# Optimization experiments

Hardware: AMD Instinct MI355X
Metric: run time of the kernel (lower is better)

Reference implementation:

```python
import jax, jax.numpy as jnp
import numpy as np
from jax import lax

B, C, T = 64, 122, 500
COUT, D, H, FF, L = 64, 128, 8, 256, 2
NSUB, NCLS = 13, 4
EPS = 1e-5


def _gelu(x):
    return jax.nn.gelu(x, approximate=False)  # torch nn.GELU default (erf)


def _bn(x, g, b, m, v):
    # eval-mode BatchNorm1d over channel dim of [N, C, T]
    scale = (g / jnp.sqrt(v + EPS))[None, :, None]
    return (x - m[None, :, None]) * scale + b[None, :, None]


def _ln(x, g, b):
    mu = x.mean(-1, keepdims=True)
    var = ((x - mu) ** 2).mean(-1, keepdims=True)
    return (x - mu) / jnp.sqrt(var + EPS) * g + b


def _conv1d(x, w, b, pad):
    y = lax.conv_general_dilated(x, w, (1,), [(pad, pad)], dimension_numbers=('NCH', 'OIH', 'NCH'))
    return y + b[None, :, None]


def forward(x, subject_ids, conv1_w, conv1_b, bn1_g, bn1_b, bn1_m, bn1_v,
            conv2_w, conv2_b, bn2_g, bn2_b, bn2_m, bn2_v,
            proj_w, proj_b, elec_emb,
            qkv_w, qkv_b, out_w, out_b, ln1_g, ln1_b,
            ff1_w, ff1_b, ff2_w, ff2_b, ln2_g, ln2_b,
            heads_w, heads_b):
    bsz = x.shape[0]
    h = x.reshape(bsz * C, 1, T)                               # [B*C, 1, T]
    h = _gelu(_bn(_conv1d(h, conv1_w, conv1_b, 4), bn1_g, bn1_b, bn1_m, bn1_v))
    h = h.reshape(bsz * C, COUT, T // 2, 2).max(-1)            # MaxPool1d(2)
    h = _gelu(_bn(_conv1d(h, conv2_w, conv2_b, 2), bn2_g, bn2_b, bn2_m, bn2_v))
    h = h.mean(-1)                                             # AdaptiveAvgPool1d(1)
    tok = h @ proj_w.T + proj_b                                # [B*C, D]
    tok = tok.reshape(bsz, C, D) + elec_emb[:, :C, :]
    dh = D // H
    inv_sqrt_dh = 1.0 / float(np.sqrt(dh))
    for l in range(L):  # post-norm TransformerEncoderLayer, gelu activation
        qkv = jnp.einsum('bsd,ed->bse', tok, qkv_w[l]) + qkv_b[l]
        q, k, v = jnp.split(qkv, 3, axis=-1)
        q = q.reshape(bsz, C, H, dh)
        k = k.reshape(bsz, C, H, dh)
        v = v.reshape(bsz, C, H, dh)
        att = jax.nn.softmax(jnp.einsum('bqhd,bkhd->bhqk', q, k) * inv_sqrt_dh, axis=-1)
        ctx = jnp.einsum('bhqk,bkhd->bqhd', att, v).reshape(bsz, C, D)
        tok = _ln(tok + ctx @ out_w[l].T + out_b[l], ln1_g[l], ln1_b[l])
        ff = _gelu(tok @ ff1_w[l].T + ff1_b[l]) @ ff2_w[l].T + ff2_b[l]
        tok = _ln(tok + ff, ln2_g[l], ln2_b[l])
    pooled = tok.mean(axis=1)                                  # [B, D]
    # per-subject head routing == gather subject's weight/bias, batched matvec
    hw = heads_w[subject_ids]                                  # [B, NCLS, D]
    hb = heads_b[subject_ids]                                  # [B, NCLS]
    return jnp.einsum('bd,bcd->bc', pooled, hw) + hb


def setup_inputs() -> dict:
    key = jax.random.key(0)
    ks = jax.random.split(key, 16)
    def n(i, shape, s=0.02):
        return jax.random.normal(ks[i], shape, jnp.float32) * s
    return {
        'x': jax.random.normal(ks[0], (B, C, T), jnp.float32),
        'subject_ids': jax.random.randint(ks[1], (B,), 0, NSUB),
        'conv1_w': n(2, (COUT, 1, 9), 0.3), 'conv1_b': jnp.zeros((COUT,), jnp.float32),
        'bn1_g': jnp.ones((COUT,), jnp.float32), 'bn1_b': jnp.zeros((COUT,), jnp.float32),
        'bn1_m': jnp.zeros((COUT,), jnp.float32), 'bn1_v': jnp.ones((COUT,), jnp.float32),
        'conv2_w': n(3, (COUT, COUT, 5), 0.05), 'conv2_b': jnp.zeros((COUT,), jnp.float32),
        'bn2_g': jnp.ones((COUT,), jnp.float32), 'bn2_b': jnp.zeros((COUT,), jnp.float32),
        'bn2_m': jnp.zeros((COUT,), jnp.float32), 'bn2_v': jnp.ones((COUT,), jnp.float32),
        'proj_w': n(4, (D, COUT), 0.05), 'proj_b': jnp.zeros((D,), jnp.float32),
        'elec_emb': n(5, (1, C, D), 0.02),
        'qkv_w': n(6, (L, 3 * D, D), 0.05), 'qkv_b': jnp.zeros((L, 3 * D), jnp.float32),
        'out_w': n(7, (L, D, D), 0.05), 'out_b': jnp.zeros((L, D), jnp.float32),
        'ln1_g': jnp.ones((L, D), jnp.float32), 'ln1_b': jnp.zeros((L, D), jnp.float32),
        'ff1_w': n(8, (L, FF, D), 0.05), 'ff1_b': jnp.zeros((L, FF), jnp.float32),
        'ff2_w': n(9, (L, D, FF), 0.05), 'ff2_b': jnp.zeros((L, D), jnp.float32),
        'ln2_g': jnp.ones((L, D), jnp.float32), 'ln2_b': jnp.zeros((L, D), jnp.float32),
        'heads_w': n(10, (NSUB, NCLS, D), 0.05), 'heads_b': jnp.zeros((NSUB, NCLS), jnp.float32),
    }


def reference(x, subject_ids, conv1_w, conv1_b, bn1_g, bn1_b, bn1_m, bn1_v,
              conv2_w, conv2_b, bn2_g, bn2_b, bn2_m, bn2_v,
              proj_w, proj_b, elec_emb,
              qkv_w, qkv_b, out_w, out_b, ln1_g, ln1_b,
              ff1_w, ff1_b, ff2_w, ff2_b, ln2_g, ln2_b,
              heads_w, heads_b):
    return forward(x, subject_ids, conv1_w, conv1_b, bn1_g, bn1_b, bn1_m, bn1_v,
                   conv2_w, conv2_b, bn2_g, bn2_b, bn2_m, bn2_v,
                   proj_w, proj_b, elec_emb,
                   qkv_w, qkv_b, out_w, out_b, ln1_g, ln1_b,
                   ff1_w, ff1_b, ff2_w, ff2_b, ln2_g, ln2_b,
                   heads_w, heads_b)
```

## Files before the change

### kernel.cpp

```cpp
#include <hip/hip_runtime.h>
#include <hip/hip_fp16.h>
#include <hip/hip_bf16.h>
#include <math.h>

#define BB 64
#define CC 122
#define TT 500
#define NCOUT 64
#define DD 128
#define HHEADS 8
#define FFDIM 256
#define NLAYER 2
#define EPS 1e-5f
#define SEQ (BB*CC)

#define WS_W2T     0u
#define WS_S1      20480u
#define WS_SH1     20544u
#define WS_S2      20608u
#define WS_SH2     20672u
#define WS_WBF     20736u
#define WS_TOK     151808u
#define WS_QKVB    1151232u
#define WS_VTB     2150656u
#define WS_GTAB    2674944u
#define WS_W1S     2675968u
#define WS_QKVB2   2676992u
#define WS_VTB2    3676416u

#define WB_QKV  0u
#define WB_OUT  98304u
#define WB_FF1  131072u
#define WB_FF2  196608u

typedef __attribute__((ext_vector_type(8))) short bf16x8;
typedef __attribute__((ext_vector_type(4))) float f32x4;

__device__ __forceinline__ unsigned short f2bf(float f) {
    unsigned int u = __float_as_uint(f);
    unsigned int r = u + 0x7FFFu + ((u >> 16) & 1u);
    return (unsigned short)(r >> 16);
}

__device__ __forceinline__ float gelu_fast(float x) {
    float z = fabsf(x) * 0.70710678118654752f;
    float t = __builtin_amdgcn_rcpf(fmaf(0.3275911f, z, 1.0f));
    float p = fmaf(fmaf(fmaf(fmaf(1.061405429f, t, -1.453152027f), t,
                             1.421413741f), t, -0.284496736f), t, 0.254829592f);
    float e = __expf(-z * z);
    float erf_abs = fmaf(-p * t, e, 1.0f);
    float erf_x = copysignf(erf_abs, x);
    return 0.5f * x * (1.0f + erf_x);
}

__device__ __forceinline__ float gelu_tab(float x, const unsigned* __restrict__ gt) {
    float p = fmaf(x, 32.0f, 256.0f);
    p = fminf(fmaxf(p, 0.0f), 511.999f);
    int i = (int)p;
    float fr = p - (float)i;
    unsigned u = gt[i];
    __half2 h2 = *(__half2*)&u;
    float v0 = __half2float(h2.x);
    float d  = __half2float(h2.y);
    return fmaf(fr, d, v0);
}

__global__ void prep_kernel(const float* __restrict__ conv1_w, const float* __restrict__ conv1_b,
                            const float* __restrict__ bn1_g, const float* __restrict__ bn1_b,
                            const float* __restrict__ bn1_m, const float* __restrict__ bn1_v,
                            const float* __restrict__ conv2_w, const float* __restrict__ conv2_b,
                            const float* __restrict__ bn2_g, const float* __restrict__ bn2_b,
                            const float* __restrict__ bn2_m, const float* __restrict__ bn2_v,
                            const float* __restrict__ qkv_w, const float* __restrict__ out_w,
                            const float* __restrict__ ff1_w, const float* __restrict__ ff2_w,
                            float* __restrict__ ws) {
    int idx = blockIdx.x * blockDim.x + threadIdx.x;
    if (idx < 20480) {
        int ci = idx & 63; int co = (idx >> 6) & 63; int kk = idx >> 12;
        unsigned short* wt = (unsigned short*)(ws + WS_W2T);
        wt[idx] = f2bf(conv2_w[(co*64 + ci)*5 + kk]);
    } else if (idx < 20544) {
        int i = idx - 20480;
        float s = bn1_g[i] * rsqrtf(bn1_v[i] + EPS);
        ws[WS_S1 + i] = s;
        ws[WS_SH1 + i] = (conv1_b[i] - bn1_m[i]) * s + bn1_b[i];
    } else if (idx < 20608) {
        int i = idx - 20544;
        float s = bn2_g[i] * rsqrtf(bn2_v[i] + EPS);
        ws[WS_S2 + i] = s;
        ws[WS_SH2 + i] = (conv2_b[i] - bn2_m[i]) * s + bn2_b[i];
    } else if (idx < 282752) {
        int r = idx - 20608;
        unsigned short* wbf = (unsigned short*)(ws + WS_WBF);
        float v;
        if (r < 98304)       v = qkv_w[r];
        else if (r < 131072) v = out_w[r - 98304];
        else if (r < 196608) v = ff1_w[r - 131072];
        else                 v = ff2_w[r - 196608];
        wbf[r] = f2bf(v);
    } else if (idx < 283264) {
        int i = idx - 282752;
        float x0 = (i - 256) * 0.03125f;
        float x1 = x0 + 0.03125f;
        float g0 = 0.5f*x0*(1.0f + erff(x0*0.70710678118654752f));
        float g1 = 0.5f*x1*(1.0f + erff(x1*0.70710678118654752f));
        __half hv = __float2half_rn(g0);
        __half hd = __float2half_rn(g1 - g0);
        unsigned short uv = *(unsigned short*)&hv;
        unsigned short ud = *(unsigned short*)&hd;
        ((unsigned*)(ws + WS_GTAB))[i] = (unsigned)uv | ((unsigned)ud << 16);
    } else if (idx < 285312) {
        int i = idx - 283264;
        int co = i >> 5, k = i & 31;
        unsigned short* w1s = (unsigned short*)(ws + WS_W1S);
        float s = bn1_g[co] * rsqrtf(bn1_v[co] + EPS);
        w1s[i] = (k < 9) ? f2bf(conv1_w[co*9 + k] * s) : (unsigned short)0;
    }
}

__global__ __launch_bounds__(256, 4) void conv_kernel(const float* __restrict__ x,
            const float* __restrict__ proj_w, const float* __restrict__ proj_b,
            const float* __restrict__ elec,
            const float* __restrict__ wsr, float* __restrict__ tok) {
    __shared__ __align__(16) unsigned short h1s[264*64];
    __shared__ __align__(16) unsigned short xbf[544];
    __shared__ __align__(16) unsigned gtab[512];
    __shared__ float part[256];
    __shared__ float mean_l[64];
    int n = blockIdx.x;
    int c = n % CC;
    int tid = threadIdx.x;
    const float* xg = x + (size_t)n * TT;

    for (int i = tid; i < 544; i += 256) {
        unsigned short v = 0;
        if (i >= 4 && i < 504) v = f2bf(xg[i-4]);
        xbf[i] = v;
    }
    if (tid < 128) {
        ((uint4*)gtab)[tid] = ((const uint4*)(wsr + WS_GTAB))[tid];
    }
    for (int idx = tid; idx < 14*64; idx += 256) {
        int rr = idx >> 6;
        int r = (rr < 2) ? rr : (rr - 2 + 252);
        h1s[r*64 + (idx & 63)] = 0;
    }
    __syncthreads();

    int lane = tid & 63;
    int w = tid >> 6;
    int ln15 = lane & 15, lg = lane >> 4;

    {
        const unsigned short* w1s = (const unsigned short*)(wsr + WS_W1S);
        bf16x8 b1f[4];
        float sh1v[4];
#pragma unroll
        for (int nt = 0; nt < 4; nt++) {
            int co = nt*16 + ln15;
            b1f[nt] = *(const bf16x8*)&w1s[co*32 + lg*8];
            sh1v[nt] = wsr[WS_SH1 + co];
        }
        for (int mi = 0; mi < 8; mi++) {
            int mt = w*8 + mi;
            int t = mt*16 + ln15;
            short e[8];
#pragma unroll
            for (int j = 0; j < 8; j++) e[j] = (short)xbf[t + lg*8 + j];
            bf16x8 af = {e[0],e[1],e[2],e[3],e[4],e[5],e[6],e[7]};
#pragma unroll
            for (int nt = 0; nt < 4; nt++) {
                f32x4 cacc = __builtin_amdgcn_mfma_f32_16x16x32_bf16(af, b1f[nt],
                                (f32x4){0.f,0.f,0.f,0.f}, 0, 0, 0);
                float g0 = gelu_tab(cacc[0] + sh1v[nt], gtab);
                float g1 = gelu_tab(cacc[1] + sh1v[nt], gtab);
                float g2 = gelu_tab(cacc[2] + sh1v[nt], gtab);
                float g3 = gelu_tab(cacc[3] + sh1v[nt], gtab);
                int tpA = mt*8 + lg*2;
                if (tpA < 250) {
                    int co = nt*16 + ln15;
                    union { __hip_bfloat162 b; unsigned u; } pk;
                    pk.b = __float22bfloat162_rn(make_float2(fmaxf(g0, g1), fmaxf(g2, g3)));
                    int r = tpA + 2;
                    int cp = (co >> 3) ^ (r & 7);
                    h1s[r*64 + cp*8 + (co & 7)] = (unsigned short)(pk.u & 0xffffu);
                    int r2 = r + 1;
                    int cp2 = (co >> 3) ^ (r2 & 7);
                    h1s[r2*64 + cp2*8 + (co & 7)] = (unsigned short)(pk.u >> 16);
                }
            }
        }
    }
    __syncthreads();

    const unsigned short* wt = (const unsigned short*)(wsr + WS_W2T);
    f32x4 acc[4][4];
#pragma unroll
    for (int mi = 0; mi < 4; mi++)
#pragma unroll
        for (int nt = 0; nt < 4; nt++) acc[mi][nt] = (f32x4){0.f, 0.f, 0.f, 0.f};

    const unsigned short* wbase = wt + ln15*64 + lg*8;
#pragma unroll
    for (int kk = 0; kk < 5; kk++) {
#pragma unroll
        for (int s = 0; s < 2; s++) {
            bf16x8 bfv[4];
#pragma unroll
            for (int nt = 0; nt < 4; nt++)
                bfv[nt] = *(const bf16x8*)(wbase + kk*4096 + nt*1024 + s*32);
#pragma unroll
            for (int mi = 0; mi < 4; mi++) {
                int r = (w*4 + mi)*16 + ln15 + kk;
                int cp = (s*4 + lg) ^ (r & 7);
                bf16x8 af = *(const bf16x8*)&h1s[r*64 + cp*8];
#pragma unroll
                for (int nt = 0; nt < 4; nt++)
                    acc[mi][nt] = __builtin_amdgcn_mfma_f32_16x16x32_bf16(af, bfv[nt], acc[mi][nt], 0, 0, 0);
            }
        }
    }

#pragma unroll
    for (int nt = 0; nt < 4; nt++) {
        int co2 = nt*16 + ln15;
        float sc = wsr[WS_S2 + co2], sh = wsr[WS_SH2 + co2];
        float p = 0.f;
#pragma unroll
        for (int mi = 0; mi < 4; mi++) {
            int tbase = (w*4 + mi)*16 + lg*4;
#pragma unroll
            for (int i = 0; i < 4; i++) {
                if (tbase + i < 250)
                    p += gelu_tab(fmaf(acc[mi][nt][i], sc, sh), gtab);
            }
        }
        p += __shfl_down(p, 32, 64);
        p += __shfl_down(p, 16, 64);
        if (lane < 16) part[w*64 + co2] = p;
    }
    __syncthreads();
    if (tid < 64) {
        mean_l[tid] = (part[tid] + part[64+tid] + part[128+tid] + part[192+tid]) * (1.0f/250.0f);
    }
    __syncthreads();

    if (tid < DD) {
        int d = tid;
        float a = proj_b[d] + elec[c*DD + d];
#pragma unroll 8
        for (int o = 0; o < 64; o++) a = fmaf(mean_l[o], proj_w[d*64 + o], a);
        tok[(size_t)n * DD + d] = a;
    }
}

__global__ __launch_bounds__(256) void qkv_gemm(const float* __restrict__ Aptr,
        const unsigned short* __restrict__ Bbf,
        const float* __restrict__ bias,
        unsigned short* __restrict__ qkvb,
        unsigned short* __restrict__ vtb) {
    const int tid = threadIdx.x;
    const int m0 = blockIdx.x * 32;
    const int y  = blockIdx.y;
    const int n0 = y * 128;
    __shared__ __align__(16) unsigned short As[32*128];

    const float* A = Aptr + (size_t)m0 * 128;
    for (int i = tid; i < 1024; i += 256) {
        int m = i >> 5; int kq = (i & 31)*4;
        float4 v = *(const float4*)(A + m*128 + kq);
        int cp = (kq >> 3) ^ (m & 15);
        short4 s4 = make_short4((short)f2bf(v.x), (short)f2bf(v.y),
                                (short)f2bf(v.z), (short)f2bf(v.w));
        *(short4*)&As[m*128 + cp*8 + (kq & 7)] = s4;
    }
    __syncthreads();

    const int lane = tid & 63, w = tid >> 6;
    const int ln15 = lane & 15, lg = lane >> 4;
    f32x4 acc[2][2];
#pragma unroll
    for (int mi = 0; mi < 2; mi++)
#pragma unroll
        for (int ni = 0; ni < 2; ni++) acc[mi][ni] = (f32x4){0.f, 0.f, 0.f, 0.f};

    const unsigned short* Bb = Bbf + (size_t)n0 * 128;
#pragma unroll
    for (int kt = 0; kt < 4; kt++) {
        bf16x8 af[2], bfv[2];
#pragma unroll
        for (int mi = 0; mi < 2; mi++) {
            int m = mi*16 + ln15;
            int cp = (kt*4 + lg) ^ (m & 15);
            af[mi] = *(const bf16x8*)&As[m*128 + cp*8];
        }
#pragma unroll
        for (int ni = 0; ni < 2; ni++) {
            int nn = (w*2 + ni)*16 + ln15;
            bfv[ni] = *(const bf16x8*)&Bb[(size_t)nn*128 + kt*32 + lg*8];
        }
#pragma unroll
        for (int mi = 0; mi < 2; mi++)
#pragma unroll
            for (int ni = 0; ni < 2; ni++)
                acc[mi][ni] = __builtin_amdgcn_mfma_f32_16x16x32_bf16(af[mi], bfv[ni], acc[mi][ni], 0, 0, 0);
    }

#pragma unroll
    for (int mi = 0; mi < 2; mi++)
#pragma unroll
        for (int ni = 0; ni < 2; ni++) {
            int nloc = (w*2 + ni)*16 + ln15;
            float bb = bias[n0 + nloc];
#pragma unroll
            for (int i = 0; i < 4; i++) {
                int ml = mi*16 + lg*4 + i;
                int nrow = m0 + ml;
                unsigned short us = f2bf(acc[mi][ni][i] + bb);
                if (y < 2) {
                    qkvb[(size_t)nrow*256 + n0 + nloc] = us;
                } else {
                    int bq = nrow / 122;
                    int j  = nrow - bq*122;
                    vtb[((size_t)(bq*128 + nloc))*128 + j] = us;
                }
            }
        }
}

__global__ __launch_bounds__(512) void attn_tail(
        const unsigned short* __restrict__ qkvb,
        const unsigned short* __restrict__ vtb,
        const unsigned short* __restrict__ outW, const float* __restrict__ outb,
        float* __restrict__ tok,
        const float* __restrict__ ln1g, const float* __restrict__ ln1b,
        const unsigned short* __restrict__ B1, const float* __restrict__ b1,
        const unsigned short* __restrict__ B2, const float* __restrict__ b2,
        const float* __restrict__ ln2g, const float* __restrict__ ln2b,
        const unsigned short* __restrict__ Bq, const float* __restrict__ bq,
        unsigned short* __restrict__ qkvb_o, unsigned short* __restrict__ vtb_o,
        int do_qkv) {
    __shared__ float Cs[32*129];
    __shared__ __align__(16) unsigned short Pregion[8*16*128];
    __shared__ __align__(16) unsigned short ctxs[32*128];

    const int tid = threadIdx.x;
    const int blk = blockIdx.x;
    const int b = blk >> 2, mq = blk & 3;
    const int m0l = mq * 32;
    const int lane = tid & 63, w = tid >> 6;
    const int ln15 = lane & 15, lg = lane >> 4;

    const unsigned short* qb = qkvb + (size_t)b * 122 * 256;
    unsigned short* Pw = Pregion + w * 2048;

    {
        const int h = w;
#pragma unroll
        for (int mt = 0; mt < 2; mt++) {
            int mrow = m0l + mt*16 + ln15;
            int gr = (mrow < 122) ? mrow : 121;
            bf16x8 af = {0,0,0,0,0,0,0,0};
            if (lg < 2) af = *(const bf16x8*)(qb + gr*256 + h*16 + lg*8);
            f32x4 S[8];
#pragma unroll
            for (int nt = 0; nt < 8; nt++) {
                int j = nt*16 + ln15;
                int gj = (j < 122) ? j : 121;
                bf16x8 bv = {0,0,0,0,0,0,0,0};
                if (lg < 2) bv = *(const bf16x8*)(qb + gj*256 + 128 + h*16 + lg*8);
                S[nt] = __builtin_amdgcn_mfma_f32_16x16x32_bf16(af, bv,
                            (f32x4){0.f,0.f,0.f,0.f}, 0, 0, 0);
            }
            float sm[4];
#pragma unroll
            for (int i = 0; i < 4; i++) {
                float m_ = -1e30f;
#pragma unroll
                for (int nt = 0; nt < 8; nt++) {
                    float v = S[nt][i] * 0.25f;
                    if (nt == 7 && ln15 >= 10) v = -1e30f;
                    S[nt][i] = v;
                    m_ = fmaxf(m_, v);
                }
                m_ = fmaxf(m_, __shfl_xor(m_, 1, 64));
                m_ = fmaxf(m_, __shfl_xor(m_, 2, 64));
                m_ = fmaxf(m_, __shfl_xor(m_, 4, 64));
                m_ = fmaxf(m_, __shfl_xor(m_, 8, 64));
                float s_ = 0.f;
#pragma unroll
                for (int nt = 0; nt < 8; nt++) {
                    float e = __expf(S[nt][i] - m_);
                    S[nt][i] = e;
                    s_ += e;
                }
                s_ += __shfl_xor(s_, 1, 64);
                s_ += __shfl_xor(s_, 2, 64);
                s_ += __shfl_xor(s_, 4, 64);
                s_ += __shfl_xor(s_, 8, 64);
                sm[i] = s_;
            }
#pragma unroll
            for (int nt = 0; nt < 8; nt++)
#pragma unroll
                for (int i = 0; i < 4; i++) {
                    int rp = lg*4 + i;
                    int j = nt*16 + ln15;
                    int cp = (j >> 3) ^ rp;
                    Pw[rp*128 + cp*8 + (j & 7)] = f2bf(S[nt][i]);
                }
            f32x4 cacc = (f32x4){0.f,0.f,0.f,0.f};
#pragma unroll
            for (int kt = 0; kt < 4; kt++) {
                bf16x8 bv = *(const bf16x8*)(vtb + ((size_t)(b*128 + h*16 + ln15))*128 + kt*32 + lg*8);
                int m = ln15;
                int cp = (kt*4 + lg) ^ m;
                bf16x8 ap = *(const bf16x8*)&Pw[m*128 + cp*8];
                cacc = __builtin_amdgcn_mfma_f32_16x16x32_bf16(ap, bv, cacc, 0, 0, 0);
            }
#pragma unroll
            for (int i = 0; i < 4; i++) {
                float inv = __builtin_amdgcn_rcpf(sm[i]);
                int rp = mt*16 + lg*4 + i;
                int ccol = h*16 + ln15;
                int cp = (ccol >> 3) ^ (rp & 15);
                ctxs[rp*128 + cp*8 + (ccol & 7)] = f2bf(cacc[i] * inv);
            }
        }
    }
    __syncthreads();

    {
        f32x4 acc[2];
#pragma unroll
        for (int mi = 0; mi < 2; mi++) acc[mi] = (f32x4){0.f,0.f,0.f,0.f};
        int nn = w*16 + ln15;
#pragma unroll
        for (int kt = 0; kt < 4; kt++) {
            bf16x8 bv = *(const bf16x8*)&outW[(size_t)nn*128 + kt*32 + lg*8];
#pragma unroll
            for (int mi = 0; mi < 2; mi++) {
                int m = mi*16 + ln15;
                int cp = (kt*4 + lg) ^ (m & 15);
                bf16x8 afm = *(const bf16x8*)&ctxs[m*128 + cp*8];
                acc[mi] = __builtin_amdgcn_mfma_f32_16x16x32_bf16(afm, bv, acc[mi], 0, 0, 0);
            }
        }
        float bb = outb[nn];
#pragma unroll
        for (int mi = 0; mi < 2; mi++)
#pragma unroll
            for (int i = 0; i < 4; i++) {
                int ml = mi*16 + lg*4 + i;
                int mrow = m0l + ml;
                int grow = b*122 + ((mrow < 122) ? mrow : 121);
                Cs[ml*129 + nn] = acc[mi][i] + bb + tok[(size_t)grow*128 + nn];
            }
    }
    __syncthreads();

    unsigned short* ln1buf = Pregion;
    unsigned short* Hs = Pregion + 4096;
    {
        int r = tid >> 4, sub = tid & 15;
        float s1 = 0.f, s2 = 0.f;
#pragma unroll
        for (int j = 0; j < 8; j++) {
            float vv = Cs[r*129 + sub*8 + j];
            s1 += vv; s2 += vv*vv;
        }
        s1 += __shfl_xor(s1, 1, 64); s2 += __shfl_xor(s2, 1, 64);
        s1 += __shfl_xor(s1, 2, 64); s2 += __shfl_xor(s2, 2, 64);
        s1 += __shfl_xor(s1, 4, 64); s2 += __shfl_xor(s2, 4, 64);
        s1 += __shfl_xor(s1, 8, 64); s2 += __shfl_xor(s2, 8, 64);
        float mu = s1 * (1.0f/128.0f);
        float var = s2 * (1.0f/128.0f) - mu*mu;
        float rstd = rsqrtf(var + EPS);
#pragma unroll
        for (int j = 0; j < 8; j++) {
            int nloc = sub*8 + j;
            float vv = (Cs[r*129 + nloc] - mu) * rstd * ln1g[nloc] + ln1b[nloc];
            Cs[r*129 + nloc] = vv;
            int cp = (nloc >> 3) ^ (r & 15);
            ln1buf[r*128 + cp*8 + (nloc & 7)] = f2bf(vv);
        }
    }
    __syncthreads();

    {
        f32x4 acc1[2][2];
#pragma unroll
        for (int mi = 0; mi < 2; mi++)
#pragma unroll
            for (int ni = 0; ni < 2; ni++) acc1[mi][ni] = (f32x4){0.f,0.f,0.f,0.f};
#pragma unroll
        for (int kt = 0; kt < 4; kt++) {
            bf16x8 afm[2];
#pragma unroll
            for (int mi = 0; mi < 2; mi++) {
                int m = mi*16 + ln15;
                int cp = (kt*4 + lg) ^ (m & 15);
                afm[mi] = *(const bf16x8*)&ln1buf[m*128 + cp*8];
            }
#pragma unroll
            for (int ni = 0; ni < 2; ni++) {
                int nn = (w*2 + ni)*16 + ln15;
                bf16x8 bv = *(const bf16x8*)&B1[(size_t)nn*128 + kt*32 + lg*8];
#pragma unroll
                for (int mi = 0; mi < 2; mi++)
                    acc1[mi][ni] = __builtin_amdgcn_mfma_f32_16x16x32_bf16(afm[mi], bv, acc1[mi][ni], 0, 0, 0);
            }
        }
#pragma unroll
        for (int ni = 0; ni < 2; ni++) {
            int nn = (w*2 + ni)*16 + ln15;
            float bb = b1[nn];
#pragma unroll
            for (int mi = 0; mi < 2; mi++)
#pragma unroll
                for (int i = 0; i < 4; i++) {
                    int m = mi*16 + lg*4 + i;
                    float v = gelu_fast(acc1[mi][ni][i] + bb);
                    int cp = (nn >> 3) ^ (m & 15);
                    Hs[m*256 + cp*8 + (nn & 7)] = f2bf(v);
                }
        }
    }
    __syncthreads();

    {
        f32x4 acc2[2];
#pragma unroll
        for (int mi = 0; mi < 2; mi++) acc2[mi] = (f32x4){0.f,0.f,0.f,0.f};
        int nn = w*16 + ln15;
#pragma unroll
        for (int kt = 0; kt < 8; kt++) {
            bf16x8 bv = *(const bf16x8*)&B2[(size_t)nn*256 + kt*32 + lg*8];
#pragma unroll
            for (int mi = 0; mi < 2; mi++) {
                int m = mi*16 + ln15;
                int cp = (kt*4 + lg) ^ (m & 15);
                bf16x8 afm = *(const bf16x8*)&Hs[m*256 + cp*8];
                acc2[mi] = __builtin_amdgcn_mfma_f32_16x16x32_bf16(afm, bv, acc2[mi], 0, 0, 0);
            }
        }
        float bb = b2[nn];
#pragma unroll
        for (int mi = 0; mi < 2; mi++)
#pragma unroll
            for (int i = 0; i < 4; i++) {
                int ml = mi*16 + lg*4 + i;
                Cs[ml*129 + nn] = acc2[mi][i] + bb + Cs[ml*129 + nn];
            }
    }
    __syncthreads();

    {
        int r = tid >> 4, sub = tid & 15;
        float s1 = 0.f, s2 = 0.f;
#pragma unroll
        for (int j = 0; j < 8; j++) {
            float vv = Cs[r*129 + sub*8 + j];
            s1 += vv; s2 += vv*vv;
        }
        s1 += __shfl_xor(s1, 1, 64); s2 += __shfl_xor(s2, 1, 64);
        s1 += __shfl_xor(s1, 2, 64); s2 += __shfl_xor(s2, 2, 64);
        s1 += __shfl_xor(s1, 4, 64); s2 += __shfl_xor(s2, 4, 64);
        s1 += __shfl_xor(s1, 8, 64); s2 += __shfl_xor(s2, 8, 64);
        float mu = s1 * (1.0f/128.0f);
        float var = s2 * (1.0f/128.0f) - mu*mu;
        float rstd = rsqrtf(var + EPS);
        bool rowok = (m0l + r < 122);
#pragma unroll
        for (int j = 0; j < 8; j++) {
            int nloc = sub*8 + j;
            float vv = (Cs[r*129 + nloc] - mu) * rstd * ln2g[nloc] + ln2b[nloc];
            if (rowok)
                tok[((size_t)(b*122 + m0l + r))*128 + nloc] = vv;
            if (do_qkv) {
                int cp = (nloc >> 3) ^ (r & 15);
                Pregion[r*128 + cp*8 + (nloc & 7)] = f2bf(vv);
            }
        }
    }

    if (do_qkv) {
        __syncthreads();
        const unsigned short* qbuf = Pregion;
        f32x4 accq[2][3];
#pragma unroll
        for (int mi = 0; mi < 2; mi++)
#pragma unroll
            for (int ni = 0; ni < 3; ni++) accq[mi][ni] = (f32x4){0.f,0.f,0.f,0.f};
#pragma unroll
        for (int kt = 0; kt < 4; kt++) {
            bf16x8 afm[2];
#pragma unroll
            for (int mi = 0; mi < 2; mi++) {
                int m = mi*16 + ln15;
                int cp = (kt*4 + lg) ^ (m & 15);
                afm[mi] = *(const bf16x8*)&qbuf[m*128 + cp*8];
            }
#pragma unroll
            for (int ni = 0; ni < 3; ni++) {
                int e = w*48 + ni*16 + ln15;
                bf16x8 bv = *(const bf16x8*)&Bq[(size_t)e*128 + kt*32 + lg*8];
#pragma unroll
                for (int mi = 0; mi < 2; mi++)
                    accq[mi][ni] = __builtin_amdgcn_mfma_f32_16x16x32_bf16(afm[mi], bv, accq[mi][ni], 0, 0, 0);
            }
        }
#pragma unroll
        for (int ni = 0; ni < 3; ni++) {
            int e = w*48 + ni*16 + ln15;
            float bb = bq[e];
#pragma unroll
            for (int mi = 0; mi < 2; mi++)
#pragma unroll
                for (int i = 0; i < 4; i++) {
                    int ml = mi*16 + lg*4 + i;
                    int mrow = m0l + ml;
                    if (mrow < 122) {
                        unsigned short us = f2bf(accq[mi][ni][i] + bb);
                        int nrow = b*122 + mrow;
                        if (e < 256)
                            qkvb_o[(size_t)nrow*256 + e] = us;
                        else
                            vtb_o[((size_t)(b*128 + (e - 256)))*128 + mrow] = us;
                    }
                }
        }
    }
}

__global__ __launch_bounds__(128) void final_kernel(const float* __restrict__ tok,
        const int* __restrict__ sid,
        const float* __restrict__ hw, const float* __restrict__ hb,
        float* __restrict__ outp) {
    __shared__ float pool[DD];
    int b = blockIdx.x, tid = threadIdx.x;
    float s = 0.f;
    for (int c2 = 0; c2 < CC; c2++) s += tok[((size_t)b*CC + c2)*DD + tid];
    pool[tid] = s * (1.0f/(float)CC);
    __syncthreads();
    if (tid < 4) {
        int sb = sid[b];
        const float* w = hw + ((size_t)sb*4 + tid)*DD;
        float a = hb[sb*4 + tid];
#pragma unroll 8
        for (int d = 0; d < DD; d++) a = fmaf(pool[d], w[d], a);
        outp[b*4 + tid] = a;
    }
}

extern "C" void kernel_launch(void* const* d_in, const int* in_sizes, int n_in,
                              void* d_out, int out_size, void* d_ws, size_t ws_size,
                              hipStream_t stream) {
    const float* x       = (const float*)d_in[0];
    const int*   sid     = (const int*)  d_in[1];
    const float* conv1_w = (const float*)d_in[2];
    const float* conv1_b = (const float*)d_in[3];
    const float* bn1_g   = (const float*)d_in[4];
    const float* bn1_b   = (const float*)d_in[5];
    const float* bn1_m   = (const float*)d_in[6];
    const float* bn1_v   = (const float*)d_in[7];
    const float* conv2_w = (const float*)d_in[8];
    const float* conv2_b = (const float*)d_in[9];
    const float* bn2_g   = (const float*)d_in[10];
    const float* bn2_b   = (const float*)d_in[11];
    const float* bn2_m   = (const float*)d_in[12];
    const float* bn2_v   = (const float*)d_in[13];
    const float* proj_w  = (const float*)d_in[14];
    const float* proj_b  = (const float*)d_in[15];
    const float* elec    = (const float*)d_in[16];
    const float* qkv_w   = (const float*)d_in[17];
    const float* qkv_b   = (const float*)d_in[18];
    const float* out_w   = (const float*)d_in[19];
    const float* out_b   = (const float*)d_in[20];
    const float* ln1_g   = (const float*)d_in[21];
    const float* ln1_b   = (const float*)d_in[22];
    const float* ff1_w   = (const float*)d_in[23];
    const float* ff1_b   = (const float*)d_in[24];
    const float* ff2_w   = (const float*)d_in[25];
    const float* ff2_b   = (const float*)d_in[26];
    const float* ln2_g   = (const float*)d_in[27];
    const float* ln2_b   = (const float*)d_in[28];
    const float* heads_w = (const float*)d_in[29];
    const float* heads_b = (const float*)d_in[30];
    float* ws = (float*)d_ws;
    const unsigned short* wbf = (const unsigned short*)(ws + WS_WBF);
    unsigned short* qkvb  = (unsigned short*)(ws + WS_QKVB);
    unsigned short* vtb   = (unsigned short*)(ws + WS_VTB);
    unsigned short* qkvb2 = (unsigned short*)(ws + WS_QKVB2);
    unsigned short* vtb2  = (unsigned short*)(ws + WS_VTB2);

    prep_kernel<<<(285312 + 255)/256, 256, 0, stream>>>(
        conv1_w, conv1_b, bn1_g, bn1_b, bn1_m, bn1_v,
        conv2_w, conv2_b, bn2_g, bn2_b, bn2_m, bn2_v,
        qkv_w, out_w, ff1_w, ff2_w, ws);

    conv_kernel<<<SEQ, 256, 0, stream>>>(x, proj_w, proj_b, elec, ws, ws + WS_TOK);

    qkv_gemm<<<dim3(244,3), 256, 0, stream>>>(
        ws + WS_TOK, wbf + WB_QKV, qkv_b, qkvb, vtb);

    attn_tail<<<BB*4, 512, 0, stream>>>(
        qkvb, vtb,
        wbf + WB_OUT, out_b,
        ws + WS_TOK, ln1_g, ln1_b,
        wbf + WB_FF1, ff1_b,
        wbf + WB_FF2, ff2_b,
        ln2_g, ln2_b,
        wbf + WB_QKV + 49152, qkv_b + 384, qkvb2, vtb2, 1);

    attn_tail<<<BB*4, 512, 0, stream>>>(
        qkvb2, vtb2,
        wbf + WB_OUT + 16384, out_b + 128,
        ws + WS_TOK, ln1_g + 128, ln1_b + 128,
        wbf + WB_FF1 + 32768, ff1_b + 256,
        wbf + WB_FF2 + 32768, ff2_b + 128,
        ln2_g + 128, ln2_b + 128,
        wbf + WB_QKV, qkv_b, qkvb2, vtb2, 0);

    final_kernel<<<BB, 128, 0, stream>>>(ws + WS_TOK, sid, heads_w, heads_b, (float*)d_out);
}
```

Measured before the change: 419.0 us.

## Restructure conv1 MFMA into even/odd pool pairs with hardware bf16 conversion

The conv1 stage now loads a register window of input once and builds even and odd shifted bf16 operands. It issues paired MFMAs so the max-pool combines matching output rows directly, instead of gathering eight scalar LDS reads per tile. The BN shift and the GELU table scale are folded into a single fma, and the h1s swizzle gains an extra XOR bit to cut LDS bank conflicts. Software round-to-nearest bf16 conversion is replaced throughout by the hardware v_cvt_pk_bf16_f32 instruction, which could differ slightly in NaN or rounding edge cases.

New measurement: 424.8 us. Within noise of the previous version (+1.4%).

```diff
diff --git a/kernel.cpp b/kernel.cpp
--- a/kernel.cpp
+++ b/kernel.cpp
@@ -42,6 +42,15 @@
     return (unsigned short)(r >> 16);
 }
 
+__device__ __forceinline__ unsigned pk_bf16(float a, float b) {
+    float r;
+    asm("v_cvt_pk_bf16_f32 %0, %1, %2" : "=v"(r) : "v"(a), "v"(b));
+    return __float_as_uint(r);
+}
+__device__ __forceinline__ unsigned short f2bf_hw(float f) {
+    return (unsigned short)pk_bf16(f, f);
+}
+
 __device__ __forceinline__ float gelu_fast(float x) {
     float z = fabsf(x) * 0.70710678118654752f;
     float t = __builtin_amdgcn_rcpf(fmaf(0.3275911f, z, 1.0f));
@@ -53,8 +62,7 @@
     return 0.5f * x * (1.0f + erf_x);
 }
 
-__device__ __forceinline__ float gelu_tab(float x, const unsigned* __restrict__ gt) {
-    float p = fmaf(x, 32.0f, 256.0f);
+__device__ __forceinline__ float gelu_idx(float p, const unsigned* __restrict__ gt) {
     p = fminf(fmaxf(p, 0.0f), 511.999f);
     int i = (int)p;
     float fr = p - (float)i;
@@ -134,7 +142,7 @@
 
     for (int i = tid; i < 544; i += 256) {
         unsigned short v = 0;
-        if (i >= 4 && i < 504) v = f2bf(xg[i-4]);
+        if (i >= 4 && i < 504) v = f2bf_hw(xg[i-4]);
         xbf[i] = v;
     }
     if (tid < 128) {
@@ -154,39 +162,46 @@
     {
         const unsigned short* w1s = (const unsigned short*)(wsr + WS_W1S);
         bf16x8 b1f[4];
-        float sh1v[4];
+        float shp[4];
 #pragma unroll
         for (int nt = 0; nt < 4; nt++) {
             int co = nt*16 + ln15;
             b1f[nt] = *(const bf16x8*)&w1s[co*32 + lg*8];
-            sh1v[nt] = wsr[WS_SH1 + co];
-        }
-        for (int mi = 0; mi < 8; mi++) {
-            int mt = w*8 + mi;
-            int t = mt*16 + ln15;
-            short e[8];
-#pragma unroll
-            for (int j = 0; j < 8; j++) e[j] = (short)xbf[t + lg*8 + j];
-            bf16x8 af = {e[0],e[1],e[2],e[3],e[4],e[5],e[6],e[7]};
+            shp[nt] = fmaf(wsr[WS_SH1 + co], 32.0f, 256.0f);
+        }
+        int P = w*128 + ln15*8 + lg*8;
+        uint4 Va = *(const uint4*)&xbf[P];
+        uint4 Vb = *(const uint4*)&xbf[P + 8];
+        unsigned vwin[8] = {Va.x, Va.y, Va.z, Va.w, Vb.x, Vb.y, Vb.z, Vb.w};
+#pragma unroll
+        for (int a = 0; a < 4; a++) {
+            union { unsigned u[4]; bf16x8 b; } Ue, Uo;
+#pragma unroll
+            for (int d = 0; d < 4; d++) {
+                Ue.u[d] = vwin[a + d];
+                Uo.u[d] = (vwin[a + d] >> 16) | (vwin[a + d + 1] << 16);
+            }
+            f32x4 ce[4], cod[4];
 #pragma unroll
             for (int nt = 0; nt < 4; nt++) {
-                f32x4 cacc = __builtin_amdgcn_mfma_f32_16x16x32_bf16(af, b1f[nt],
-                                (f32x4){0.f,0.f,0.f,0.f}, 0, 0, 0);
-                float g0 = gelu_tab(cacc[0] + sh1v[nt], gtab);
-                float g1 = gelu_tab(cacc[1] + sh1v[nt], gtab);
-                float g2 = gelu_tab(cacc[2] + sh1v[nt], gtab);
-                float g3 = gelu_tab(cacc[3] + sh1v[nt], gtab);
-                int tpA = mt*8 + lg*2;
-                if (tpA < 250) {
-                    int co = nt*16 + ln15;
-                    union { __hip_bfloat162 b; unsigned u; } pk;
-                    pk.b = __float22bfloat162_rn(make_float2(fmaxf(g0, g1), fmaxf(g2, g3)));
-                    int r = tpA + 2;
-                    int cp = (co >> 3) ^ (r & 7);
-                    h1s[r*64 + cp*8 + (co & 7)] = (unsigned short)(pk.u & 0xffffu);
-                    int r2 = r + 1;
-                    int cp2 = (co >> 3) ^ (r2 & 7);
-                    h1s[r2*64 + cp2*8 + (co & 7)] = (unsigned short)(pk.u >> 16);
+                ce[nt]  = __builtin_amdgcn_mfma_f32_16x16x32_bf16(Ue.b, b1f[nt],
+                              (f32x4){0.f,0.f,0.f,0.f}, 0, 0, 0);
+                cod[nt] = __builtin_amdgcn_mfma_f32_16x16x32_bf16(Uo.b, b1f[nt],
+                              (f32x4){0.f,0.f,0.f,0.f}, 0, 0, 0);
+            }
+#pragma unroll
+            for (int nt = 0; nt < 4; nt++) {
+                int co = nt*16 + ln15;
+#pragma unroll
+                for (int i = 0; i < 4; i++) {
+                    int tp = w*64 + lg*16 + i*4 + a;
+                    if (tp < 250) {
+                        float ge = gelu_idx(fmaf(ce[nt][i],  32.0f, shp[nt]), gtab);
+                        float go = gelu_idx(fmaf(cod[nt][i], 32.0f, shp[nt]), gtab);
+                        int r = tp + 2;
+                        int cp = (co >> 3) ^ (r & 7) ^ (((r >> 4) & 1) << 1);
+                        h1s[r*64 + cp*8 + (co & 7)] = f2bf_hw(fmaxf(ge, go));
+                    }
                 }
             }
         }
@@ -212,7 +227,7 @@
 #pragma unroll
             for (int mi = 0; mi < 4; mi++) {
                 int r = (w*4 + mi)*16 + ln15 + kk;
-                int cp = (s*4 + lg) ^ (r & 7);
+                int cp = (s*4 + lg) ^ (r & 7) ^ (((r >> 4) & 1) << 1);
                 bf16x8 af = *(const bf16x8*)&h1s[r*64 + cp*8];
 #pragma unroll
                 for (int nt = 0; nt < 4; nt++)
@@ -224,7 +239,8 @@
 #pragma unroll
     for (int nt = 0; nt < 4; nt++) {
         int co2 = nt*16 + ln15;
-        float sc = wsr[WS_S2 + co2], sh = wsr[WS_SH2 + co2];
+        float sc = wsr[WS_S2 + co2] * 32.0f;
+        float sh = fmaf(wsr[WS_SH2 + co2], 32.0f, 256.0f);
         float p = 0.f;
 #pragma unroll
         for (int mi = 0; mi < 4; mi++) {
@@ -232,7 +248,7 @@
 #pragma unroll
             for (int i = 0; i < 4; i++) {
                 if (tbase + i < 250)
-                    p += gelu_tab(fmaf(acc[mi][nt][i], sc, sh), gtab);
+                    p += gelu_idx(fmaf(acc[mi][nt][i], sc, sh), gtab);
             }
         }
         p += __shfl_down(p, 32, 64);
@@ -270,9 +286,9 @@
         int m = i >> 5; int kq = (i & 31)*4;
         float4 v = *(const float4*)(A + m*128 + kq);
         int cp = (kq >> 3) ^ (m & 15);
-        short4 s4 = make_short4((short)f2bf(v.x), (short)f2bf(v.y),
-                                (short)f2bf(v.z), (short)f2bf(v.w));
-        *(short4*)&As[m*128 + cp*8 + (kq & 7)] = s4;
+        unsigned p0 = pk_bf16(v.x, v.y);
+        unsigned p1 = pk_bf16(v.z, v.w);
+        *(uint2*)&As[m*128 + cp*8 + (kq & 7)] = make_uint2(p0, p1);
     }
     __syncthreads();
 
@@ -316,7 +332,7 @@
             for (int i = 0; i < 4; i++) {
                 int ml = mi*16 + lg*4 + i;
                 int nrow = m0 + ml;
-                unsigned short us = f2bf(acc[mi][ni][i] + bb);
+                unsigned short us = f2bf_hw(acc[mi][ni][i] + bb);
                 if (y < 2) {
                     qkvb[(size_t)nrow*256 + n0 + nloc] = us;
                 } else {
@@ -407,7 +423,7 @@
                     int rp = lg*4 + i;
                     int j = nt*16 + ln15;
                     int cp = (j >> 3) ^ rp;
-                    Pw[rp*128 + cp*8 + (j & 7)] = f2bf(S[nt][i]);
+                    Pw[rp*128 + cp*8 + (j & 7)] = f2bf_hw(S[nt][i]);
                 }
             f32x4 cacc = (f32x4){0.f,0.f,0.f,0.f};
 #pragma unroll
@@ -424,7 +440,7 @@
                 int rp = mt*16 + lg*4 + i;
                 int ccol = h*16 + ln15;
                 int cp = (ccol >> 3) ^ (rp & 15);
-                ctxs[rp*128 + cp*8 + (ccol & 7)] = f2bf(cacc[i] * inv);
+                ctxs[rp*128 + cp*8 + (ccol & 7)] = f2bf_hw(cacc[i] * inv);
             }
         }
     }
@@ -482,7 +498,7 @@
             float vv = (Cs[r*129 + nloc] - mu) * rstd * ln1g[nloc] + ln1b[nloc];
             Cs[r*129 + nloc] = vv;
             int cp = (nloc >> 3) ^ (r & 15);
-            ln1buf[r*128 + cp*8 + (nloc & 7)] = f2bf(vv);
+            ln1buf[r*128 + cp*8 + (nloc & 7)] = f2bf_hw(vv);
         }
     }
     __syncthreads();
@@ -522,7 +538,7 @@
                     int m = mi*16 + lg*4 + i;
                     float v = gelu_fast(acc1[mi][ni][i] + bb);
                     int cp = (nn >> 3) ^ (m & 15);
-                    Hs[m*256 + cp*8 + (nn & 7)] = f2bf(v);
+                    Hs[m*256 + cp*8 + (nn & 7)] = f2bf_hw(v);
                 }
         }
     }
@@ -579,7 +595,7 @@
                 tok[((size_t)(b*122 + m0l + r))*128 + nloc] = vv;
             if (do_qkv) {
                 int cp = (nloc >> 3) ^ (r & 15);
-                Pregion[r*128 + cp*8 + (nloc & 7)] = f2bf(vv);
+                Pregion[r*128 + cp*8 + (nloc & 7)] = f2bf_hw(vv);
             }
         }
     }
@@ -621,7 +637,7 @@
                     int ml = mi*16 + lg*4 + i;
                     int mrow = m0l + ml;
                     if (mrow < 122) {
-                        unsigned short us = f2bf(accq[mi][ni][i] + bb);
+                        unsigned short us = f2bf_hw(accq[mi][ni][i] + bb);
                         int nrow = b*122 + mrow;
                         if (e < 256)
                             qkvb_o[(size_t)nrow*256 + e] = us;
```
